# Optimization experiments

Hardware: AMD Instinct MI355X
Metric: run time of the kernel (lower is better)

## Reference

```python
import jax, jax.numpy as jnp
import numpy as np

Q_DIM, KV_DIM, H = 64, 64, 4


def setup_inputs() -> dict:
    key = jax.random.key(0)
    ks = jax.random.split(key, 8)
    b, t = 8, 128
    q_x = jax.random.normal(ks[0], (b, t, Q_DIM), dtype=jnp.float32)
    kv_x = jax.random.normal(ks[1], (b, t, t - 1, KV_DIM), dtype=jnp.float32)
    # nn.Linear weights: (out_features, in_features), applied as x @ W.T
    Wk = jax.random.normal(ks[2], (KV_DIM * H, KV_DIM), dtype=jnp.float32) * 0.05
    Wq = jax.random.normal(ks[3], (KV_DIM * H, Q_DIM), dtype=jnp.float32) * 0.05
    Wv = jax.random.normal(ks[4], (KV_DIM * H, KV_DIM), dtype=jnp.float32) * 0.05
    bias = jax.random.uniform(ks[5], (KV_DIM,), minval=-0.1, maxval=0.1, dtype=jnp.float32)
    Ws = jax.random.normal(ks[6], (1, KV_DIM), dtype=jnp.float32) * 0.05
    bs = jax.random.normal(ks[7], (1,), dtype=jnp.float32) * 0.05
    return {"q_x": q_x, "kv_x": kv_x, "Wk": Wk, "Wq": Wq, "Wv": Wv,
            "bias": bias, "Ws": Ws, "bs": bs}


def reference(q_x, kv_x, Wk, Wq, Wv, bias, Ws, bs):
    b, t, tm1, k = kv_x.shape  # tm1 == t-1
    h = H
    # keys: (b, t, t-1, h, k)
    keys = (kv_x @ Wk.T).reshape(b, t, tm1, h, k)
    # queries: (b, t, 1, h, k)
    queries = (q_x @ Wq.T).reshape(b, t, 1, h, k)
    # additive tanh score projected to scalar per (b,t,n,h)
    act = jnp.tanh(keys + queries + bias)
    score = jnp.einsum('btnhk,k->btnh', act, Ws[0]) + bs[0]
    # softmax over the t-1 key axis (dim=2)
    w = jax.nn.softmax(score, axis=2)  # (b, t, t-1, h)
    values = (kv_x @ Wv.T).reshape(b, t, tm1, h, k)
    # weighted sum over t-1
    x = jnp.einsum('btnh,btnhk->bthk', w, values)
    return x.reshape(b, t, h * k)
```

## Files before the change

kernel.cpp:

```cpp
#include <hip/hip_runtime.h>
#include <math.h>

#define B 8
#define T 128
#define NKEY 127
#define NPAD 128
#define KDIM 64
#define NH 4
#define CH 256

typedef short short8 __attribute__((ext_vector_type(8)));
typedef float floatx4 __attribute__((ext_vector_type(4)));

__device__ __forceinline__ float fast_tanh(float x) {
    float e = __expf(2.f * x);
    float r = __builtin_amdgcn_rcpf(e + 1.f);
    return fmaf(-2.f, r, 1.f);
}

__device__ __forceinline__ void split8(const float4& a, const float4& b,
                                       short8& hi, short8& lo) {
    float x[8] = {a.x, a.y, a.z, a.w, b.x, b.y, b.z, b.w};
    #pragma unroll
    for (int i = 0; i < 8; ++i) {
        unsigned u = __float_as_uint(x[i]);
        hi[i] = (short)(u >> 16);
        float l = x[i] - __uint_as_float(u & 0xFFFF0000u);
        lo[i] = (short)(__float_as_uint(l) >> 16);
    }
}

__global__ __launch_bounds__(256, 4)
void attn_kernel(const float* __restrict__ q_x,
                 const float* __restrict__ kv_x,
                 const float* __restrict__ Wk,
                 const float* __restrict__ Wq,
                 const float* __restrict__ Wv,
                 const float* __restrict__ bias,
                 const float* __restrict__ Ws,
                 const float* __restrict__ bs,
                 float* __restrict__ out)
{
    __shared__ __align__(16) short bh_lds[16][64][8];
    __shared__ __align__(16) short bl_lds[16][64][8];
    __shared__ float qb_lds[CH];
    __shared__ float p_lds[NH][NPAD];
    __shared__ float wkv_lds[NH][KDIM];

    const int bt   = blockIdx.x;
    const int tid  = threadIdx.x;
    const int h    = tid >> 6;
    const int lane = tid & 63;
    const int col  = lane & 15;
    const int quad = lane >> 4;

    const float* __restrict__ kvg = kv_x + (size_t)bt * NKEY * KDIM;

    #pragma unroll
    for (int w = 0; w < 4; ++w) {
        const int chunk = w * 4 + h;
        const int nt = chunk >> 1, ks = chunk & 1;
        const int n  = nt * 16 + (lane & 15);
        const int k0 = ks * 32 + (lane >> 4) * 8;
        float4 a = make_float4(0.f, 0.f, 0.f, 0.f);
        float4 b = make_float4(0.f, 0.f, 0.f, 0.f);
        if (n < NKEY) {
            const float* p = kvg + (size_t)n * KDIM + k0;
            a = *(const float4*)p;
            b = *(const float4*)(p + 4);
        }
        short8 hi, lo;
        split8(a, b, hi, lo);
        *(short8*)&bh_lds[chunk][lane][0] = hi;
        *(short8*)&bl_lds[chunk][lane][0] = lo;
    }

    {
        const float4* Wq4 = (const float4*)(Wq + (size_t)tid * KDIM);
        const float4* q4g = (const float4*)(q_x + (size_t)bt * KDIM);
        float4 qa = {0.f, 0.f, 0.f, 0.f};
        #pragma unroll
        for (int i = 0; i < 16; ++i) {
            float4 w = Wq4[i];
            float4 q4 = q4g[i];
            qa.x = fmaf(q4.x, w.x, qa.x);
            qa.y = fmaf(q4.y, w.y, qa.y);
            qa.z = fmaf(q4.z, w.z, qa.z);
            qa.w = fmaf(q4.w, w.w, qa.w);
        }
        qb_lds[tid] = (qa.x + qa.y) + (qa.z + qa.w) + bias[tid & 63];
    }

    short8 ahi[4][2], alo[4][2];
    #pragma unroll
    for (int jt = 0; jt < 4; ++jt)
        #pragma unroll
        for (int ks = 0; ks < 2; ++ks) {
            const float* wrow = Wk + (size_t)(h * 64 + jt * 16 + col) * KDIM
                                   + ks * 32 + quad * 8;
            float4 a = *(const float4*)wrow;
            float4 b = *(const float4*)(wrow + 4);
            split8(a, b, ahi[jt][ks], alo[jt][ks]);
        }

    __syncthreads();

    float qbv[4][4], wsv[4][4];
    #pragma unroll
    for (int jt = 0; jt < 4; ++jt)
        #pragma unroll
        for (int r = 0; r < 4; ++r) {
            int j = jt * 16 + quad * 4 + r;
            qbv[jt][r] = qb_lds[h * 64 + j];
            wsv[jt][r] = Ws[j];
        }

    for (int nt = 0; nt < 8; ++nt) {
        short8 bhi0 = *(const short8*)&bh_lds[nt * 2 + 0][lane][0];
        short8 blo0 = *(const short8*)&bl_lds[nt * 2 + 0][lane][0];
        short8 bhi1 = *(const short8*)&bh_lds[nt * 2 + 1][lane][0];
        short8 blo1 = *(const short8*)&bl_lds[nt * 2 + 1][lane][0];

        floatx4 acc[4];
        #pragma unroll
        for (int jt = 0; jt < 4; ++jt) {
            floatx4 c = {0.f, 0.f, 0.f, 0.f};
            c = __builtin_amdgcn_mfma_f32_16x16x32_bf16(ahi[jt][0], bhi0, c, 0, 0, 0);
            c = __builtin_amdgcn_mfma_f32_16x16x32_bf16(ahi[jt][1], bhi1, c, 0, 0, 0);
            c = __builtin_amdgcn_mfma_f32_16x16x32_bf16(ahi[jt][0], blo0, c, 0, 0, 0);
            c = __builtin_amdgcn_mfma_f32_16x16x32_bf16(ahi[jt][1], blo1, c, 0, 0, 0);
            c = __builtin_amdgcn_mfma_f32_16x16x32_bf16(alo[jt][0], bhi0, c, 0, 0, 0);
            c = __builtin_amdgcn_mfma_f32_16x16x32_bf16(alo[jt][1], bhi1, c, 0, 0, 0);
            acc[jt] = c;
        }

        float partial = 0.f;
        #pragma unroll
        for (int jt = 0; jt < 4; ++jt)
            #pragma unroll
            for (int r = 0; r < 4; ++r)
                partial = fmaf(fast_tanh(acc[jt][r] + qbv[jt][r]), wsv[jt][r], partial);
        partial += __shfl_xor(partial, 16, 64);
        partial += __shfl_xor(partial, 32, 64);
        if (lane < 16) p_lds[h][nt * 16 + lane] = partial;
    }

    float invl;
    {
        float s_a = p_lds[h][lane];
        float s_b = p_lds[h][64 + lane];
        if (lane == 63) s_b = -1e30f;
        float mx = fmaxf(s_a, s_b);
        #pragma unroll
        for (int off = 32; off > 0; off >>= 1)
            mx = fmaxf(mx, __shfl_xor(mx, off, 64));
        float pa = __expf(s_a - mx);
        float pb = __expf(s_b - mx);
        float ls = pa + pb;
        #pragma unroll
        for (int off = 32; off > 0; off >>= 1)
            ls += __shfl_xor(ls, off, 64);
        invl = 1.f / ls;
        p_lds[h][lane]      = pa;
        p_lds[h][64 + lane] = pb;
    }

    {
        float w0 = 0.f, w1 = 0.f, w2 = 0.f, w3 = 0.f;
        #pragma unroll 8
        for (int n4 = 0; n4 < NPAD; n4 += 4) {
            float4 p4 = *(const float4*)&p_lds[h][n4];
            const int n3 = (n4 + 3 < NKEY) ? (n4 + 3) : 0;
            w0 = fmaf(p4.x, kvg[(size_t)(n4 + 0) * KDIM + lane], w0);
            w1 = fmaf(p4.y, kvg[(size_t)(n4 + 1) * KDIM + lane], w1);
            w2 = fmaf(p4.z, kvg[(size_t)(n4 + 2) * KDIM + lane], w2);
            w3 = fmaf(p4.w, kvg[(size_t)n3 * KDIM + lane], w3);
        }
        wkv_lds[h][lane] = ((w0 + w1) + (w2 + w3)) * invl;
    }

    {
        const float4* Wv4 = (const float4*)(Wv + (size_t)tid * KDIM);
        const float4* wv_row = (const float4*)wkv_lds[h];
        float4 oa = {0.f, 0.f, 0.f, 0.f};
        #pragma unroll
        for (int i = 0; i < 16; ++i) {
            float4 w = Wv4[i];
            float4 c = wv_row[i];
            oa.x = fmaf(c.x, w.x, oa.x);
            oa.y = fmaf(c.y, w.y, oa.y);
            oa.z = fmaf(c.z, w.z, oa.z);
            oa.w = fmaf(c.w, w.w, oa.w);
        }
        out[(size_t)bt * CH + tid] = (oa.x + oa.y) + (oa.z + oa.w);
    }
}

extern "C" void kernel_launch(void* const* d_in, const int* in_sizes, int n_in,
                              void* d_out, int out_size, void* d_ws, size_t ws_size,
                              hipStream_t stream) {
    const float* q_x  = (const float*)d_in[0];
    const float* kv_x = (const float*)d_in[1];
    const float* Wk   = (const float*)d_in[2];
    const float* Wq   = (const float*)d_in[3];
    const float* Wv   = (const float*)d_in[4];
    const float* bias = (const float*)d_in[5];
    const float* Ws   = (const float*)d_in[6];
    const float* bs   = (const float*)d_in[7];
    float* out = (float*)d_out;

    attn_kernel<<<dim3(B * T), dim3(256), 0, stream>>>(
        q_x, kv_x, Wk, Wq, Wv, bias, Ws, bs, out);
}
```

Measured before the change: 127.0 us.

## Preload kv rows into registers and split weighted sum across warps by key

Each wave now loads a 32-key slice of kv_x into registers at kernel start and later computes partial weighted sums for all four heads over that slice. The partials go through a new LDS buffer and are reduced per head. Before, each head's wave re-read all 127 kv rows from global/L2 after the softmax. This removes four redundant reads of the same data and moves the load off the critical path, at the cost of 32 extra registers per thread, more LDS, and two extra block barriers, which may hurt occupancy.

```diff
diff --git a/kernel.cpp b/kernel.cpp
--- a/kernel.cpp
+++ b/kernel.cpp
@@ -45,6 +45,7 @@
     __shared__ __align__(16) short bl_lds[16][64][8];
     __shared__ float qb_lds[CH];
     __shared__ float p_lds[NH][NPAD];
+    __shared__ float part_lds[NH][NH][KDIM];
     __shared__ float wkv_lds[NH][KDIM];
 
     const int bt   = blockIdx.x;
@@ -55,6 +56,13 @@
     const int quad = lane >> 4;
 
     const float* __restrict__ kvg = kv_x + (size_t)bt * NKEY * KDIM;
+
+    float kvreg[32];
+    #pragma unroll
+    for (int i = 0; i < 32; ++i) {
+        const int n = 32 * h + i;
+        kvreg[i] = (n < NKEY) ? kvg[(size_t)n * KDIM + lane] : 0.f;
+    }
 
     #pragma unroll
     for (int w = 0; w < 4; ++w) {
@@ -165,19 +173,30 @@
         p_lds[h][64 + lane] = pb;
     }
 
-    {
-        float w0 = 0.f, w1 = 0.f, w2 = 0.f, w3 = 0.f;
-        #pragma unroll 8
-        for (int n4 = 0; n4 < NPAD; n4 += 4) {
-            float4 p4 = *(const float4*)&p_lds[h][n4];
-            const int n3 = (n4 + 3 < NKEY) ? (n4 + 3) : 0;
-            w0 = fmaf(p4.x, kvg[(size_t)(n4 + 0) * KDIM + lane], w0);
-            w1 = fmaf(p4.y, kvg[(size_t)(n4 + 1) * KDIM + lane], w1);
-            w2 = fmaf(p4.z, kvg[(size_t)(n4 + 2) * KDIM + lane], w2);
-            w3 = fmaf(p4.w, kvg[(size_t)n3 * KDIM + lane], w3);
-        }
-        wkv_lds[h][lane] = ((w0 + w1) + (w2 + w3)) * invl;
-    }
+    __syncthreads();
+
+    {
+        float part[NH] = {0.f, 0.f, 0.f, 0.f};
+        #pragma unroll
+        for (int i4 = 0; i4 < 32; i4 += 4) {
+            #pragma unroll
+            for (int h2 = 0; h2 < NH; ++h2) {
+                float4 p4 = *(const float4*)&p_lds[h2][32 * h + i4];
+                part[h2] = fmaf(p4.x, kvreg[i4 + 0],
+                           fmaf(p4.y, kvreg[i4 + 1],
+                           fmaf(p4.z, kvreg[i4 + 2],
+                           fmaf(p4.w, kvreg[i4 + 3], part[h2]))));
+            }
+        }
+        #pragma unroll
+        for (int h2 = 0; h2 < NH; ++h2)
+            part_lds[h2][h][lane] = part[h2];
+    }
+
+    __syncthreads();
+
+    wkv_lds[h][lane] = (part_lds[h][0][lane] + part_lds[h][1][lane]
+                      + part_lds[h][2][lane] + part_lds[h][3][lane]) * invl;
 
     {
         const float4* Wv4 = (const float4*)(Wv + (size_t)tid * KDIM);
```

New measurement: 151.6 us. 1.19x slower.

## Stage kv tile as padded fp32 in LDS and reuse it for value reduction

Applied to the files above, without the earlier changes.

The kv_x tile is now staged in LDS as padded fp32 rows (pitch 68) instead of pre-split bf16 hi/lo fragments. Each wave splits the B operand on the fly per tile, and the Wk fragments are processed in two passes of two j-tiles to cut register pressure. The weighted value sum now reads kv from LDS with float4 loads instead of re-reading global memory, followed by a cross-quad shuffle reduction. The cost is repeated hi/lo split work in the inner loop (done twice per tile) and a larger LDS footprint, which may limit occupancy.

```diff
diff --git a/kernel.cpp b/kernel.cpp
--- a/kernel.cpp
+++ b/kernel.cpp
@@ -8,6 +8,7 @@
 #define KDIM 64
 #define NH 4
 #define CH 256
+#define PITCH 68
 
 typedef short short8 __attribute__((ext_vector_type(8)));
 typedef float floatx4 __attribute__((ext_vector_type(4)));
@@ -41,11 +42,10 @@
                  const float* __restrict__ bs,
                  float* __restrict__ out)
 {
-    __shared__ __align__(16) short bh_lds[16][64][8];
-    __shared__ __align__(16) short bl_lds[16][64][8];
+    __shared__ __align__(16) float kv_f[NPAD * PITCH];
     __shared__ float qb_lds[CH];
     __shared__ float p_lds[NH][NPAD];
-    __shared__ float wkv_lds[NH][KDIM];
+    __shared__ __align__(16) float wkv_lds[NH][KDIM];
 
     const int bt   = blockIdx.x;
     const int tid  = threadIdx.x;
@@ -57,22 +57,13 @@
     const float* __restrict__ kvg = kv_x + (size_t)bt * NKEY * KDIM;
 
     #pragma unroll
-    for (int w = 0; w < 4; ++w) {
-        const int chunk = w * 4 + h;
-        const int nt = chunk >> 1, ks = chunk & 1;
-        const int n  = nt * 16 + (lane & 15);
-        const int k0 = ks * 32 + (lane >> 4) * 8;
-        float4 a = make_float4(0.f, 0.f, 0.f, 0.f);
-        float4 b = make_float4(0.f, 0.f, 0.f, 0.f);
-        if (n < NKEY) {
-            const float* p = kvg + (size_t)n * KDIM + k0;
-            a = *(const float4*)p;
-            b = *(const float4*)(p + 4);
-        }
-        short8 hi, lo;
-        split8(a, b, hi, lo);
-        *(short8*)&bh_lds[chunk][lane][0] = hi;
-        *(short8*)&bl_lds[chunk][lane][0] = lo;
+    for (int i = 0; i < 8; ++i) {
+        const int g  = i * 256 + tid;
+        const int n  = g >> 4;
+        const int kk = g & 15;
+        float4 v = make_float4(0.f, 0.f, 0.f, 0.f);
+        if (n < NKEY) v = ((const float4*)kvg)[g];
+        *(float4*)&kv_f[n * PITCH + kk * 4] = v;
     }
 
     {
@@ -91,58 +82,72 @@
         qb_lds[tid] = (qa.x + qa.y) + (qa.z + qa.w) + bias[tid & 63];
     }
 
-    short8 ahi[4][2], alo[4][2];
-    #pragma unroll
-    for (int jt = 0; jt < 4; ++jt)
-        #pragma unroll
-        for (int ks = 0; ks < 2; ++ks) {
-            const float* wrow = Wk + (size_t)(h * 64 + jt * 16 + col) * KDIM
-                                   + ks * 32 + quad * 8;
-            float4 a = *(const float4*)wrow;
-            float4 b = *(const float4*)(wrow + 4);
-            split8(a, b, ahi[jt][ks], alo[jt][ks]);
-        }
-
     __syncthreads();
 
-    float qbv[4][4], wsv[4][4];
-    #pragma unroll
-    for (int jt = 0; jt < 4; ++jt)
-        #pragma unroll
-        for (int r = 0; r < 4; ++r) {
-            int j = jt * 16 + quad * 4 + r;
-            qbv[jt][r] = qb_lds[h * 64 + j];
-            wsv[jt][r] = Ws[j];
-        }
-
+    float spartial[8] = {0.f, 0.f, 0.f, 0.f, 0.f, 0.f, 0.f, 0.f};
+
+    #pragma unroll
+    for (int pass = 0; pass < 2; ++pass) {
+        short8 ahi[2][2], alo[2][2];
+        float qbp[2][4], wsp[2][4];
+        #pragma unroll
+        for (int jj = 0; jj < 2; ++jj) {
+            const int jt = 2 * pass + jj;
+            #pragma unroll
+            for (int ks = 0; ks < 2; ++ks) {
+                const float* wrow = Wk + (size_t)(h * 64 + jt * 16 + col) * KDIM
+                                       + ks * 32 + quad * 8;
+                float4 a = *(const float4*)wrow;
+                float4 b = *(const float4*)(wrow + 4);
+                split8(a, b, ahi[jj][ks], alo[jj][ks]);
+            }
+            #pragma unroll
+            for (int r = 0; r < 4; ++r) {
+                const int j = jt * 16 + quad * 4 + r;
+                qbp[jj][r] = qb_lds[h * 64 + j];
+                wsp[jj][r] = Ws[j];
+            }
+        }
+
+        for (int nt = 0; nt < 8; ++nt) {
+            short8 bhi[2], blo[2];
+            #pragma unroll
+            for (int ks = 0; ks < 2; ++ks) {
+                const float* p = &kv_f[(nt * 16 + col) * PITCH + ks * 32 + quad * 8];
+                float4 a = *(const float4*)p;
+                float4 b = *(const float4*)(p + 4);
+                split8(a, b, bhi[ks], blo[ks]);
+            }
+
+            floatx4 acc[2];
+            #pragma unroll
+            for (int jj = 0; jj < 2; ++jj) {
+                floatx4 c = {0.f, 0.f, 0.f, 0.f};
+                c = __builtin_amdgcn_mfma_f32_16x16x32_bf16(ahi[jj][0], bhi[0], c, 0, 0, 0);
+                c = __builtin_amdgcn_mfma_f32_16x16x32_bf16(ahi[jj][1], bhi[1], c, 0, 0, 0);
+                c = __builtin_amdgcn_mfma_f32_16x16x32_bf16(ahi[jj][0], blo[0], c, 0, 0, 0);
+                c = __builtin_amdgcn_mfma_f32_16x16x32_bf16(ahi[jj][1], blo[1], c, 0, 0, 0);
+                c = __builtin_amdgcn_mfma_f32_16x16x32_bf16(alo[jj][0], bhi[0], c, 0, 0, 0);
+                c = __builtin_amdgcn_mfma_f32_16x16x32_bf16(alo[jj][1], bhi[1], c, 0, 0, 0);
+                acc[jj] = c;
+            }
+
+            float part = spartial[nt];
+            #pragma unroll
+            for (int jj = 0; jj < 2; ++jj)
+                #pragma unroll
+                for (int r = 0; r < 4; ++r)
+                    part = fmaf(fast_tanh(acc[jj][r] + qbp[jj][r]), wsp[jj][r], part);
+            spartial[nt] = part;
+        }
+    }
+
+    #pragma unroll
     for (int nt = 0; nt < 8; ++nt) {
-        short8 bhi0 = *(const short8*)&bh_lds[nt * 2 + 0][lane][0];
-        short8 blo0 = *(const short8*)&bl_lds[nt * 2 + 0][lane][0];
-        short8 bhi1 = *(const short8*)&bh_lds[nt * 2 + 1][lane][0];
-        short8 blo1 = *(const short8*)&bl_lds[nt * 2 + 1][lane][0];
-
-        floatx4 acc[4];
-        #pragma unroll
-        for (int jt = 0; jt < 4; ++jt) {
-            floatx4 c = {0.f, 0.f, 0.f, 0.f};
-            c = __builtin_amdgcn_mfma_f32_16x16x32_bf16(ahi[jt][0], bhi0, c, 0, 0, 0);
-            c = __builtin_amdgcn_mfma_f32_16x16x32_bf16(ahi[jt][1], bhi1, c, 0, 0, 0);
-            c = __builtin_amdgcn_mfma_f32_16x16x32_bf16(ahi[jt][0], blo0, c, 0, 0, 0);
-            c = __builtin_amdgcn_mfma_f32_16x16x32_bf16(ahi[jt][1], blo1, c, 0, 0, 0);
-            c = __builtin_amdgcn_mfma_f32_16x16x32_bf16(alo[jt][0], bhi0, c, 0, 0, 0);
-            c = __builtin_amdgcn_mfma_f32_16x16x32_bf16(alo[jt][1], bhi1, c, 0, 0, 0);
-            acc[jt] = c;
-        }
-
-        float partial = 0.f;
-        #pragma unroll
-        for (int jt = 0; jt < 4; ++jt)
-            #pragma unroll
-            for (int r = 0; r < 4; ++r)
-                partial = fmaf(fast_tanh(acc[jt][r] + qbv[jt][r]), wsv[jt][r], partial);
-        partial += __shfl_xor(partial, 16, 64);
-        partial += __shfl_xor(partial, 32, 64);
-        if (lane < 16) p_lds[h][nt * 16 + lane] = partial;
+        float s = spartial[nt];
+        s += __shfl_xor(s, 16, 64);
+        s += __shfl_xor(s, 32, 64);
+        if (lane < 16) p_lds[h][nt * 16 + lane] = s;
     }
 
     float invl;
@@ -166,17 +171,28 @@
     }
 
     {
-        float w0 = 0.f, w1 = 0.f, w2 = 0.f, w3 = 0.f;
-        #pragma unroll 8
-        for (int n4 = 0; n4 < NPAD; n4 += 4) {
-            float4 p4 = *(const float4*)&p_lds[h][n4];
-            const int n3 = (n4 + 3 < NKEY) ? (n4 + 3) : 0;
-            w0 = fmaf(p4.x, kvg[(size_t)(n4 + 0) * KDIM + lane], w0);
-            w1 = fmaf(p4.y, kvg[(size_t)(n4 + 1) * KDIM + lane], w1);
-            w2 = fmaf(p4.z, kvg[(size_t)(n4 + 2) * KDIM + lane], w2);
-            w3 = fmaf(p4.w, kvg[(size_t)n3 * KDIM + lane], w3);
-        }
-        wkv_lds[h][lane] = ((w0 + w1) + (w2 + w3)) * invl;
+        float4 a4 = make_float4(0.f, 0.f, 0.f, 0.f);
+        #pragma unroll 4
+        for (int i = 0; i < 32; ++i) {
+            const int n = 4 * i + quad;
+            float4 v = *(const float4*)&kv_f[n * PITCH + 4 * col];
+            float pn = p_lds[h][n];
+            a4.x = fmaf(pn, v.x, a4.x);
+            a4.y = fmaf(pn, v.y, a4.y);
+            a4.z = fmaf(pn, v.z, a4.z);
+            a4.w = fmaf(pn, v.w, a4.w);
+        }
+        #pragma unroll
+        for (int off = 16; off <= 32; off <<= 1) {
+            a4.x += __shfl_xor(a4.x, off, 64);
+            a4.y += __shfl_xor(a4.y, off, 64);
+            a4.z += __shfl_xor(a4.z, off, 64);
+            a4.w += __shfl_xor(a4.w, off, 64);
+        }
+        if (lane < 16) {
+            float4 r = make_float4(a4.x * invl, a4.y * invl, a4.z * invl, a4.w * invl);
+            *(float4*)&wkv_lds[h][4 * col] = r;
+        }
     }
 
     {
```

New measurement: 151.1 us. 1.19x slower.
